# Kernel tuning notes

Measured on AMD Instinct MI355X. Metric: run time of the kernel, lower is better.

## Reference

```python
import jax, jax.numpy as jnp
import numpy as np

N = 100000
MAX_HOPS = 3
EPS = 1e-16


def _gat_conv(x, src, dst, W, a_src, a_dst, bias, heads, out_c, concat):
    """PyG-style GATConv (eval mode, self-loops, negative_slope=0.2)."""
    n = x.shape[0]
    loop = jnp.arange(n, dtype=src.dtype)
    s = jnp.concatenate([src, loop])
    d = jnp.concatenate([dst, loop])
    h = (x @ W).reshape(n, heads, out_c)                      # [N,H,C]
    al_s = (h * a_src).sum(-1)                                # [N,H]
    al_d = (h * a_dst).sum(-1)                                # [N,H]
    e = jax.nn.leaky_relu(al_s[s] + al_d[d], 0.2)             # [E,H]
    e_max = jax.ops.segment_max(e, d, num_segments=n)
    e = jnp.exp(e - e_max[d])
    denom = jax.ops.segment_sum(e, d, num_segments=n)
    alpha = e / (denom[d] + EPS)                              # edge softmax per dst
    out = jax.ops.segment_sum(h[s] * alpha[:, :, None], d, num_segments=n)  # [N,H,C]
    out = out.reshape(n, heads * out_c) if concat else out.mean(axis=1)
    return out + bias


def _hierarchy(src, dst, seed, n, max_hops):
    """BFS hop distance from seeds; one-hot rows, all-zero if unreached."""
    reached = seed
    dist = jnp.where(seed, 0, max_hops + 1)
    for h in range(1, max_hops + 1):
        msg = jax.ops.segment_max(reached[src].astype(jnp.int32), dst, num_segments=n)
        nbr = msg > 0
        dist = jnp.where(nbr & (~reached), h, dist)
        reached = reached | nbr
    mask = (dist[:, None] == jnp.arange(max_hops + 1)[None, :]).astype(jnp.float32)
    hop_counts = jnp.argmax(mask, axis=1).astype(jnp.float32)  # all-zero row -> 0, like torch
    return mask, hop_counts


def setup_inputs() -> dict:
    key = jax.random.key(0)
    ks = jax.random.split(key, 20)
    in_aug = 128 + MAX_HOPS + 1  # 132
    out_channels = 40
    g = lambda k, shp: (jax.random.normal(k, shp, dtype=jnp.float32) * 0.1)
    return {
        "x": jax.random.normal(ks[0], (N, 128), dtype=jnp.float32),
        "edge_index": jax.random.randint(ks[1], (2, 1600000), 0, N, dtype=jnp.int64),
        "seed_mask": jax.random.randint(ks[2], (N,), 0, 100, dtype=jnp.int32),
        "W1": g(ks[3], (in_aug, 8 * 8)), "a1s": g(ks[4], (8, 8)), "a1d": g(ks[5], (8, 8)), "b1": jnp.zeros((64,), jnp.float32),
        "W2": g(ks[6], (64, 8 * 16)), "a2s": g(ks[7], (8, 16)), "a2d": g(ks[8], (8, 16)), "b2": jnp.zeros((128,), jnp.float32),
        "W3": g(ks[9], (128, out_channels)), "a3s": g(ks[10], (1, out_channels)), "a3d": g(ks[11], (1, out_channels)), "b3": jnp.zeros((out_channels,), jnp.float32),
        "Wg": g(ks[12], (129, 1)), "bg": jnp.zeros((1,), jnp.float32),
    }


def reference(x, edge_index, seed_mask, W1, a1s, a1d, b1, W2, a2s, a2d, b2,
              W3, a3s, a3d, b3, Wg, bg):
    src, dst = edge_index[0], edge_index[1]
    seed = seed_mask == 0
    hmask, hop_counts = _hierarchy(src, dst, seed, N, MAX_HOPS)
    aug = jnp.concatenate([x, hmask], axis=1)
    h1 = jax.nn.elu(_gat_conv(aug, src, dst, W1, a1s, a1d, b1, 8, 8, True))
    h2 = _gat_conv(h1, src, dst, W2, a2s, a2d, b2, 8, 16, True)
    gate_in = jnp.concatenate([h2, hop_counts[:, None]], axis=1)
    gate = jax.nn.sigmoid(gate_in @ Wg + bg)
    h2 = h2 * gate
    h3 = _gat_conv(h2, src, dst, W3, a3s, a3d, b3, 1, 40, False)
    return jax.nn.log_softmax(h3, axis=1)
```

## Files before the change

### kernel.cpp

```cpp
#include <hip/hip_runtime.h>
#include <hip/hip_bf16.h>
#include <hip/hip_fp16.h>
#include <math.h>

#define MAXH 3
#define NSB 8
#define NS (1 << NSB)
#define SRCBITS 17
#define SRCMASK ((1 << SRCBITS) - 1)
#define LOG2E 1.4426950408889634f
typedef unsigned int u32;
typedef unsigned long long u64;
typedef unsigned char u8;
typedef unsigned short u16;

using bf16x8 = __attribute__((ext_vector_type(8))) short;
using f32x4  = __attribute__((ext_vector_type(4))) float;

__device__ __forceinline__ float fexp2(float x) {
#if __has_builtin(__builtin_amdgcn_exp2f)
    return __builtin_amdgcn_exp2f(x);
#else
    return exp2f(x);
#endif
}
__device__ __forceinline__ u16 f2bf(float f) {
    u32 u = __float_as_uint(f);
    u32 r = ((u >> 16) & 1u) + 0x7fffu;
    return (u16)((u + r) >> 16);
}

__global__ void k_init(const int* __restrict__ seed_mask, int* dist, u64* rb64,
                       int* bincnt, int n) {
    int i = blockIdx.x * 256 + threadIdx.x;
    int lane = threadIdx.x & 63;
    bool seed = (i < n) && (seed_mask[i] == 0);
    if (i < n) dist[i] = seed ? 0 : (MAXH + 1);
    u64 b = __ballot(seed);
    if (lane == 0 && (i & ~63) < n) rb64[i >> 6] = b;
    if (blockIdx.x == 0) {
        bincnt[threadIdx.x] = 0;
        bincnt[threadIdx.x + 256] = 0;
    }
}

__global__ void k_bfs_step(const int* __restrict__ rowptr, const int* __restrict__ csr_src,
                           const u32* __restrict__ rbOld, u64* rbNew, int* dist,
                           int h, int n) {
    int i = blockIdx.x * 256 + threadIdx.x;
    int lane = threadIdx.x & 63;
    bool reached = false;
    if (i < n) {
        reached = (rbOld[i >> 5] >> (i & 31)) & 1u;
        if (!reached) {
            int beg = rowptr[i], end = rowptr[i + 1];
            for (int k = beg; k < end; k++) {
                int s = csr_src[k];
                if ((rbOld[s >> 5] >> (s & 31)) & 1u) { reached = true; dist[i] = h; break; }
            }
        }
    }
    u64 b = __ballot(reached);
    if (lane == 0 && (i & ~63) < n) rbNew[i >> 6] = b;
}

__global__ void k_bincount(const int4* __restrict__ dst4, int* bincnt, int E4) {
    __shared__ int cnt[512];
    int t = threadIdx.x;
    cnt[t] = 0; cnt[t + 256] = 0;
    __syncthreads();
    int i = blockIdx.x * 256 + t;
    if (i < E4) {
        int4 d = dst4[i];
        atomicAdd(&cnt[d.x >> NSB], 1);
        atomicAdd(&cnt[d.y >> NSB], 1);
        atomicAdd(&cnt[d.z >> NSB], 1);
        atomicAdd(&cnt[d.w >> NSB], 1);
    }
    __syncthreads();
    if (cnt[t] > 0) atomicAdd(&bincnt[t], cnt[t]);
    if (cnt[t + 256] > 0) atomicAdd(&bincnt[t + 256], cnt[t + 256]);
}

__global__ void k_binscan(const int* __restrict__ bincnt, int* binbase, int* bincur,
                          int* rowptr, int BINS, int E, int n) {
    __shared__ int sd[512];
    int t = threadIdx.x;
    int v = (t < BINS) ? bincnt[t] : 0;
    sd[t] = v;
    __syncthreads();
    for (int off = 1; off < 512; off <<= 1) {
        int add = (t >= off) ? sd[t - off] : 0;
        __syncthreads();
        sd[t] += add;
        __syncthreads();
    }
    int excl = sd[t] - v;
    if (t < BINS) { binbase[t] = excl; bincur[t] = excl; }
    if (t == 0) { binbase[BINS] = E; rowptr[n] = E; }
}

__global__ void k_binscatter(const int4* __restrict__ src4, const int4* __restrict__ dst4,
                             int* bincur, int* __restrict__ pairs, int E4, int BINS) {
    __shared__ int cnt[512], base[512];
    int t = threadIdx.x;
    cnt[t] = 0; cnt[t + 256] = 0;
    __syncthreads();
    int i = blockIdx.x * 256 + t;
    int bin[4], rank[4], pack[4];
    bool valid = i < E4;
    if (valid) {
        int4 s = src4[i], d = dst4[i];
        bin[0] = d.x >> NSB; pack[0] = ((d.x & (NS - 1)) << SRCBITS) | s.x;
        bin[1] = d.y >> NSB; pack[1] = ((d.y & (NS - 1)) << SRCBITS) | s.y;
        bin[2] = d.z >> NSB; pack[2] = ((d.z & (NS - 1)) << SRCBITS) | s.z;
        bin[3] = d.w >> NSB; pack[3] = ((d.w & (NS - 1)) << SRCBITS) | s.w;
        rank[0] = atomicAdd(&cnt[bin[0]], 1);
        rank[1] = atomicAdd(&cnt[bin[1]], 1);
        rank[2] = atomicAdd(&cnt[bin[2]], 1);
        rank[3] = atomicAdd(&cnt[bin[3]], 1);
    }
    __syncthreads();
    if (cnt[t] > 0) base[t] = atomicAdd(&bincur[t], cnt[t]);
    if (cnt[t + 256] > 0) base[t + 256] = atomicAdd(&bincur[t + 256], cnt[t + 256]);
    __syncthreads();
    if (valid) {
        pairs[base[bin[0]] + rank[0]] = pack[0];
        pairs[base[bin[1]] + rank[1]] = pack[1];
        pairs[base[bin[2]] + rank[2]] = pack[2];
        pairs[base[bin[3]] + rank[3]] = pack[3];
    }
}

__global__ void k_binsort(const int* __restrict__ pairs, const int* __restrict__ binbase,
                          int* __restrict__ rowptr, int* __restrict__ csr_src, int n) {
    __shared__ int hist[NS];
    const int b = blockIdx.x, t = threadIdx.x;
    const int nbeg = b << NSB;
    const int ebeg = binbase[b];
    const int ecnt = binbase[b + 1] - ebeg;
    hist[t] = 0;
    __syncthreads();
    for (int i = t; i < ecnt; i += 256)
        atomicAdd(&hist[(u32)pairs[ebeg + i] >> SRCBITS], 1);
    for (int d = 1; d < NS; d <<= 1) {
        __syncthreads();
        int idx = (t + 1) * (d << 1) - 1;
        if (idx < NS) hist[idx] += hist[idx - d];
    }
    __syncthreads();
    if (t == 0) hist[NS - 1] = 0;
    for (int d = NS / 2; d >= 1; d >>= 1) {
        __syncthreads();
        int idx = (t + 1) * (d << 1) - 1;
        if (idx < NS) { int tmp = hist[idx - d]; hist[idx - d] = hist[idx]; hist[idx] += tmp; }
    }
    __syncthreads();
    int g0 = nbeg + t;
    if (g0 < n) rowptr[g0] = ebeg + hist[t];
    __syncthreads();
    for (int i = t; i < ecnt; i += 256) {
        int p = pairs[ebeg + i];
        int pos = atomicAdd(&hist[(u32)p >> SRCBITS], 1);
        csr_src[ebeg + pos] = p & SRCMASK;
    }
}

template <int SK, int MBW>
__launch_bounds__(256)
__global__ void k_gemm_mfma1(const float* __restrict__ A, const float* __restrict__ W,
                             const float* __restrict__ a_s, const float* __restrict__ a_d,
                             const int* __restrict__ dist, __half* __restrict__ out,
                             float* __restrict__ als, float* __restrict__ ald, int n) {
    constexpr int K = 128, NREAL = 64, NTT = 5, AH = 8, C = 8;
    constexpr int KT = K / 32;
    constexpr int NTCOL = (NTT - 1) * 16;
    __shared__ u16 WT[NTT * 16 * SK];
    __shared__ u16 sAW[4][16 * SK];
    __shared__ float sAug[4][64];
    __shared__ float sAugA[4][16];

    for (int idx = threadIdx.x; idx < NTT * 16 * K; idx += 256) {
        int c = idx / K, k = idx % K;
        float v;
        if (c < NREAL) {
            v = W[k * NREAL + c];
        } else {
            int j = (c - NTCOL) & 7;
            const float* aw = (c < NTCOL + AH) ? a_s : a_d;
            float accv = 0.0f;
            for (int cc = 0; cc < C; cc++) accv += W[k * NREAL + j * C + cc] * aw[j * C + cc];
            v = accv * LOG2E;
        }
        WT[c * SK + k] = f2bf(v);
    }
    {
        int t = threadIdx.x;
        int d = t >> 6, c = t & 63;
        sAug[d][c] = W[(K + d) * NREAL + c];
        if (t < 64) {
            int dd = t >> 4, j = t & 15;
            int hh = j & 7;
            const float* aw = (j < 8) ? a_s : a_d;
            float accv = 0.0f;
            for (int cc = 0; cc < C; cc++)
                accv += W[(K + dd) * NREAL + hh * C + cc] * aw[hh * C + cc];
            sAugA[dd][j] = accv * LOG2E;
        }
    }
    __syncthreads();

    const int lane = threadIdx.x & 63;
    const int l15 = lane & 15;
    const int kg = lane >> 4;
    const int w = threadIdx.x >> 6;
    const int wid = blockIdx.x * 4 + w;

    bf16x8 bfr[NTT][KT];
#pragma unroll
    for (int nt = 0; nt < NTT; nt++)
#pragma unroll
        for (int kt = 0; kt < KT; kt++)
            bfr[nt][kt] = *(const bf16x8*)&WT[(nt * 16 + l15) * SK + kt * 32 + kg * 8];

    for (int mb = 0; mb < MBW; mb++) {
        const int rowbase = (wid * MBW + mb) * 16;
        if (rowbase >= n) break;
        {
            int r = lane >> 2, c4b = lane & 3;
            const float* xr = A + (size_t)(rowbase + r) * K;
#pragma unroll
            for (int j = 0; j < 8; j++) {
                int c4 = c4b + j * 4;
                float4 v = *(const float4*)&xr[c4 * 4];
                ushort4 o;
                o.x = f2bf(v.x); o.y = f2bf(v.y); o.z = f2bf(v.z); o.w = f2bf(v.w);
                *(ushort4*)&sAW[w][r * SK + c4 * 4] = o;
            }
        }
        bf16x8 af[KT];
#pragma unroll
        for (int kt = 0; kt < KT; kt++)
            af[kt] = *(const bf16x8*)&sAW[w][l15 * SK + kt * 32 + kg * 8];
        f32x4 acc[NTT];
#pragma unroll
        for (int nt = 0; nt < NTT; nt++) acc[nt] = f32x4{0.f, 0.f, 0.f, 0.f};
#pragma unroll
        for (int kt = 0; kt < KT; kt++)
#pragma unroll
            for (int nt = 0; nt < NTT; nt++)
                acc[nt] = __builtin_amdgcn_mfma_f32_16x16x32_bf16(af[kt], bfr[nt][kt],
                                                                  acc[nt], 0, 0, 0);
        int rows[4], dd[4];
#pragma unroll
        for (int r = 0; r < 4; r++) {
            rows[r] = rowbase + kg * 4 + r;
            dd[r] = dist[rows[r]];
        }
#pragma unroll
        for (int nt = 0; nt < NTT - 1; nt++) {
            int c = nt * 16 + l15;
#pragma unroll
            for (int r = 0; r < 4; r++) {
                float v = acc[nt][r];
                if (dd[r] <= MAXH) v += sAug[dd[r]][c];
                out[(size_t)rows[r] * NREAL + c] = __float2half(v);
            }
        }
#pragma unroll
        for (int r = 0; r < 4; r++) {
            float v = acc[NTT - 1][r];
            if (dd[r] <= MAXH) v += sAugA[dd[r]][l15];
            if (l15 < AH) als[(size_t)rows[r] * AH + l15] = v;
            else ald[(size_t)rows[r] * AH + (l15 - AH)] = v;
        }
    }
}

template <int K, int NREAL, int NTT, int AH, int C, int SK, int MBW>
__launch_bounds__(256)
__global__ void k_gemm_mfma(const u16* __restrict__ A, const float* __restrict__ W,
                            const float* __restrict__ a_s, const float* __restrict__ a_d,
                            __half* __restrict__ out, float* __restrict__ als,
                            float* __restrict__ ald, int n) {
    constexpr int KT = K / 32;
    constexpr int NTCOL = (NTT - 1) * 16;
    __shared__ u16 WT[NTT * 16 * SK];
    for (int idx = threadIdx.x; idx < NTT * 16 * K; idx += 256) {
        int c = idx / K, k = idx % K;
        float v = 0.0f;
        if (c < NREAL) {
            v = W[k * NREAL + c];
        } else if (c >= NTCOL && c < NTCOL + 2 * AH) {
            int j = (c - NTCOL) % AH;
            const float* aw = (c < NTCOL + AH) ? a_s : a_d;
            float accv = 0.0f;
            for (int cc = 0; cc < C; cc++) accv += W[k * NREAL + j * C + cc] * aw[j * C + cc];
            v = accv * LOG2E;
        }
        WT[c * SK + k] = f2bf(v);
    }
    __syncthreads();

    const int lane = threadIdx.x & 63;
    const int l15 = lane & 15;
    const int kg = lane >> 4;
    const int wid = blockIdx.x * 4 + (threadIdx.x >> 6);

    bf16x8 bfr[NTT][KT];
#pragma unroll
    for (int nt = 0; nt < NTT; nt++)
#pragma unroll
        for (int kt = 0; kt < KT; kt++)
            bfr[nt][kt] = *(const bf16x8*)&WT[(nt * 16 + l15) * SK + kt * 32 + kg * 8];

    for (int mb = 0; mb < MBW; mb++) {
        const int rowbase = (wid * MBW + mb) * 16;
        if (rowbase >= n) break;
        bf16x8 af[KT];
#pragma unroll
        for (int kt = 0; kt < KT; kt++)
            af[kt] = *(const bf16x8*)&A[(size_t)(rowbase + l15) * K + kt * 32 + kg * 8];
        f32x4 acc[NTT];
#pragma unroll
        for (int nt = 0; nt < NTT; nt++) acc[nt] = f32x4{0.f, 0.f, 0.f, 0.f};
#pragma unroll
        for (int kt = 0; kt < KT; kt++)
#pragma unroll
            for (int nt = 0; nt < NTT; nt++)
                acc[nt] = __builtin_amdgcn_mfma_f32_16x16x32_bf16(af[kt], bfr[nt][kt],
                                                                  acc[nt], 0, 0, 0);
#pragma unroll
        for (int nt = 0; nt < NTT - 1; nt++) {
            int c = nt * 16 + l15;
            if (c < NREAL) {
#pragma unroll
                for (int r = 0; r < 4; r++) {
                    int row = rowbase + kg * 4 + r;
                    out[(size_t)row * NREAL + c] = __float2half(acc[nt][r]);
                }
            }
        }
#pragma unroll
        for (int r = 0; r < 4; r++) {
            int row = rowbase + kg * 4 + r;
            float v = acc[NTT - 1][r];
            if (l15 < AH) als[(size_t)row * AH + l15] = v;
            else if (l15 < 2 * AH) ald[(size_t)row * AH + (l15 - AH)] = v;
        }
    }
}

template <int H, int C, int CH, int MODE, typename OT>
__launch_bounds__(1024)
__global__ void k_gat(const int* __restrict__ rowptr, const int* __restrict__ csr_src,
                      const __half* __restrict__ h, const float* __restrict__ als,
                      const float* __restrict__ ald, const float* __restrict__ bias,
                      const int* __restrict__ dist, const float* __restrict__ Wg,
                      const float* __restrict__ bg, OT* __restrict__ out, int n) {
    constexpr int TOT = H * C;
    constexpr int NL = TOT / CH;
    const int lane = threadIdx.x & 63;
    const int node = blockIdx.x * 16 + (threadIdx.x >> 6);
    if (node >= n) return;
    const int beg = rowptr[node];
    const int deg = rowptr[node + 1] - beg;

    const int cl = (lane < NL) ? lane : 0;
    const int hd = (cl * CH) / C;
    const float ald_hd = ald[(size_t)node * H + hd];
    const float t0 = als[(size_t)node * H + hd] + ald_hd;
    const float m0 = fmaxf(t0, 0.2f * t0);
    const float c0 = ald_hd - m0;
    const float c1 = 0.2f * ald_hd - m0;

    float s = 1.0f;
    float ax = 0.0f, ay = 0.0f;
    __half2 acc2;
    if (MODE == 2) {
        acc2 = *(const __half2*)(h + (size_t)node * TOT + cl * 2);
    } else {
        ax = __half2float(h[(size_t)node * TOT + cl]);
    }

    auto body = [&](int sN) {
        float a = als[(size_t)sN * H + hd];
        float v = fmaxf(a + c0, fmaf(a, 0.2f, c1));
        float p = fexp2(v);
        s += p;
        if (MODE == 2) {
            __half2 ph = __float2half2_rn(p);
            acc2 = __hfma2(ph, *(const __half2*)(h + (size_t)sN * TOT + cl * 2), acc2);
        } else {
            ax += p * __half2float(h[(size_t)sN * TOT + cl]);
        }
    };

    for (int base = 0; base < deg; base += 64) {
        const int myE = base + lane;
        int sReg = (myE < deg) ? csr_src[beg + myE] : 0;
        const int cnt = min(64, deg - base);
        int e = 0;
        for (; e + 4 <= cnt; e += 4) {
            body(__builtin_amdgcn_readlane(sReg, e));
            body(__builtin_amdgcn_readlane(sReg, e + 1));
            body(__builtin_amdgcn_readlane(sReg, e + 2));
            body(__builtin_amdgcn_readlane(sReg, e + 3));
        }
        for (; e < cnt; e++) body(__builtin_amdgcn_readlane(sReg, e));
    }

    const float inv = 1.0f / (s + 1e-16f);
    if (MODE == 2) {
        float2 av = __half22float2(acc2);
        ax = av.x; ay = av.y;
    }
    float vx = ax * inv + bias[cl * CH];
    float vy = (CH == 2) ? (ay * inv + bias[cl * CH + 1]) : 0.0f;

    if (MODE == 1) {
        vx = vx > 0.0f ? vx : expm1f(vx);
        ((u16*)out)[(size_t)node * TOT + cl] = f2bf(vx);
    } else if (MODE == 2) {
        float2 wg = *(const float2*)&Wg[cl * 2];
        float part = vx * wg.x + vy * wg.y;
#pragma unroll
        for (int off = 32; off > 0; off >>= 1) part += __shfl_xor(part, off);
        int d = dist[node];
        float hop = (d <= MAXH) ? (float)d : 0.0f;
        float g = 1.0f / (1.0f + __expf(-(part + hop * Wg[128] + bg[0])));
        ushort2 wv;
        wv.x = f2bf(vx * g);
        wv.y = f2bf(vy * g);
        *(ushort2*)&((u16*)out)[(size_t)node * TOT + cl * 2] = wv;
    } else if (MODE == 3) {
        float v = (lane < NL) ? vx : -INFINITY;
        float mm = v;
#pragma unroll
        for (int off = 32; off > 0; off >>= 1) mm = fmaxf(mm, __shfl_xor(mm, off));
        float ex = (lane < NL) ? __expf(v - mm) : 0.0f;
        float ss = ex;
#pragma unroll
        for (int off = 32; off > 0; off >>= 1) ss += __shfl_xor(ss, off);
        float ls = logf(ss);
        if (lane < NL) ((float*)out)[(size_t)node * TOT + cl] = v - mm - ls;
    }
}

static inline int nblk(long long t, int b) { return (int)((t + b - 1) / b); }

extern "C" void kernel_launch(void* const* d_in, const int* in_sizes, int n_in,
                              void* d_out, int out_size, void* d_ws, size_t ws_size,
                              hipStream_t stream) {
    const float* x = (const float*)d_in[0];
    const int* eidx = (const int*)d_in[1];
    const int* seed_mask = (const int*)d_in[2];
    const float* W1 = (const float*)d_in[3];
    const float* a1s = (const float*)d_in[4];
    const float* a1d = (const float*)d_in[5];
    const float* b1 = (const float*)d_in[6];
    const float* W2 = (const float*)d_in[7];
    const float* a2s = (const float*)d_in[8];
    const float* a2d = (const float*)d_in[9];
    const float* b2 = (const float*)d_in[10];
    const float* W3 = (const float*)d_in[11];
    const float* a3s = (const float*)d_in[12];
    const float* a3d = (const float*)d_in[13];
    const float* b3 = (const float*)d_in[14];
    const float* Wg = (const float*)d_in[15];
    const float* bg = (const float*)d_in[16];

    const int n = in_sizes[0] / 128;
    const long long E = in_sizes[1] / 2;
    const int E4 = (int)(E / 4);
    const int4* src4 = (const int4*)eidx;
    const int4* dst4 = (const int4*)(eidx + E);
    const int BINS = (n + NS - 1) >> NSB;
    const int NW64 = (n + 63) / 64;

    char* ws = (char*)d_ws;
    size_t off = 0;
    auto alloc = [&](size_t bytes) -> void* {
        void* p = ws + off;
        off = (off + bytes + 255) & ~(size_t)255;
        return p;
    };
    int* dist    = (int*)alloc((size_t)n * 4);
    u64* rbA     = (u64*)alloc((size_t)NW64 * 8);
    u64* rbB     = (u64*)alloc((size_t)NW64 * 8);
    int* rowptr  = (int*)alloc((size_t)(n + 1) * 4);
    int* bincnt  = (int*)alloc(512 * 4);
    int* binbase = (int*)alloc(513 * 4);
    int* bincur  = (int*)alloc(512 * 4);
    int* csr_src = (int*)alloc((size_t)E * 4);
    float* als   = (float*)alloc((size_t)n * 8 * 4);
    float* ald   = (float*)alloc((size_t)n * 8 * 4);
    __half* hbuf = (__half*)alloc((size_t)n * 128 * 2);
    u16* abuf    = (u16*)alloc((size_t)n * 128 * 2);
    int* pairs   = (int*)abuf;
    float* out = (float*)d_out;

    const int BS = 256;

    k_init<<<nblk(n, BS), BS, 0, stream>>>(seed_mask, dist, rbA, bincnt, n);

    k_bincount<<<nblk(E4, BS), BS, 0, stream>>>(dst4, bincnt, E4);
    k_binscan<<<1, 512, 0, stream>>>(bincnt, binbase, bincur, rowptr, BINS, (int)E, n);
    k_binscatter<<<nblk(E4, BS), BS, 0, stream>>>(src4, dst4, bincur, pairs, E4, BINS);
    k_binsort<<<BINS, 256, 0, stream>>>(pairs, binbase, rowptr, csr_src, n);

    k_bfs_step<<<nblk(n, BS), BS, 0, stream>>>(rowptr, csr_src, (const u32*)rbA, rbB,
                                               dist, 1, n);
    k_bfs_step<<<nblk(n, BS), BS, 0, stream>>>(rowptr, csr_src, (const u32*)rbB, rbA,
                                               dist, 2, n);
    k_bfs_step<<<nblk(n, BS), BS, 0, stream>>>(rowptr, csr_src, (const u32*)rbA, rbB,
                                               dist, 3, n);

    const int mblocks = (n + 15) / 16;
    const int gmf = (mblocks + 15) / 16;

    k_gemm_mfma1<136, 4>
        <<<gmf, 256, 0, stream>>>(x, W1, a1s, a1d, dist, hbuf, als, ald, n);
    k_gat<8, 8, 1, 1, u16><<<nblk(n, 16), 1024, 0, stream>>>(
        rowptr, csr_src, hbuf, als, ald, b1, nullptr, nullptr, nullptr, abuf, n);

    k_gemm_mfma<64, 128, 9, 8, 16, 72, 4>
        <<<gmf, 256, 0, stream>>>(abuf, W2, a2s, a2d, hbuf, als, ald, n);
    k_gat<8, 16, 2, 2, u16><<<nblk(n, 16), 1024, 0, stream>>>(
        rowptr, csr_src, hbuf, als, ald, b2, dist, Wg, bg, abuf, n);

    k_gemm_mfma<128, 40, 4, 1, 40, 136, 4>
        <<<gmf, 256, 0, stream>>>(abuf, W3, a3s, a3d, hbuf, als, ald, n);
    k_gat<1, 40, 1, 3, float><<<nblk(n, 16), 1024, 0, stream>>>(
        rowptr, csr_src, hbuf, als, ald, b3, nullptr, nullptr, nullptr, out, n);
}
```

Measured before the change: 441.5 us.

## Process multiple edges per wavefront in GAT aggregation with wider per-lane channels

The GAT aggregation kernel now splits each 64-lane wavefront into edge groups (2 or 3) so that idle lanes process different neighbor edges concurrently. Each lane also handles 2 or 4 channels with vector loads, and partial sums are combined across groups with shuffles before the epilogue. Block size drops from 1024 to 256 threads with launch bounds set for higher occupancy. The binscatter kernel moves to 1024-thread blocks to reduce global atomics on the bin cursors. Extra shuffle reductions and predicated invalid edges add some overhead.

```diff
diff --git a/kernel.cpp b/kernel.cpp
--- a/kernel.cpp
+++ b/kernel.cpp
@@ -100,13 +100,14 @@
     if (t == 0) { binbase[BINS] = E; rowptr[n] = E; }
 }
 
+__launch_bounds__(1024)
 __global__ void k_binscatter(const int4* __restrict__ src4, const int4* __restrict__ dst4,
                              int* bincur, int* __restrict__ pairs, int E4, int BINS) {
     __shared__ int cnt[512], base[512];
     int t = threadIdx.x;
-    cnt[t] = 0; cnt[t + 256] = 0;
-    __syncthreads();
-    int i = blockIdx.x * 256 + t;
+    if (t < 512) cnt[t] = 0;
+    __syncthreads();
+    int i = blockIdx.x * 1024 + t;
     int bin[4], rank[4], pack[4];
     bool valid = i < E4;
     if (valid) {
@@ -121,8 +122,7 @@
         rank[3] = atomicAdd(&cnt[bin[3]], 1);
     }
     __syncthreads();
-    if (cnt[t] > 0) base[t] = atomicAdd(&bincur[t], cnt[t]);
-    if (cnt[t + 256] > 0) base[t + 256] = atomicAdd(&bincur[t + 256], cnt[t + 256]);
+    if (t < 512 && cnt[t] > 0) base[t] = atomicAdd(&bincur[t], cnt[t]);
     __syncthreads();
     if (valid) {
         pairs[base[bin[0]] + rank[0]] = pack[0];
@@ -351,8 +351,8 @@
     }
 }
 
-template <int H, int C, int CH, int MODE, typename OT>
-__launch_bounds__(1024)
+template <int H, int C, int CH, int EPP, int MODE, typename OT>
+__launch_bounds__(256, 8)
 __global__ void k_gat(const int* __restrict__ rowptr, const int* __restrict__ csr_src,
                       const __half* __restrict__ h, const float* __restrict__ als,
                       const float* __restrict__ ald, const float* __restrict__ bias,
@@ -361,12 +361,13 @@
     constexpr int TOT = H * C;
     constexpr int NL = TOT / CH;
     const int lane = threadIdx.x & 63;
-    const int node = blockIdx.x * 16 + (threadIdx.x >> 6);
+    const int node = blockIdx.x * 4 + (threadIdx.x >> 6);
     if (node >= n) return;
     const int beg = rowptr[node];
     const int deg = rowptr[node + 1] - beg;
 
-    const int cl = (lane < NL) ? lane : 0;
+    const int eg = lane / NL;
+    const int cl = lane % NL;
     const int hd = (cl * CH) / C;
     const float ald_hd = ald[(size_t)node * H + hd];
     const float t0 = als[(size_t)node * H + hd] + ald_hd;
@@ -374,76 +375,129 @@
     const float c0 = ald_hd - m0;
     const float c1 = 0.2f * ald_hd - m0;
 
-    float s = 1.0f;
+    float s = (eg == 0) ? 1.0f : 0.0f;
     float ax = 0.0f, ay = 0.0f;
-    __half2 acc2;
-    if (MODE == 2) {
-        acc2 = *(const __half2*)(h + (size_t)node * TOT + cl * 2);
-    } else {
-        ax = __half2float(h[(size_t)node * TOT + cl]);
-    }
-
-    auto body = [&](int sN) {
+    __half2 accLo = __floats2half2_rn(0.f, 0.f), accHi = accLo;
+    if (eg == 0) {
+        if (MODE == 2) {
+            uint2 hv = *(const uint2*)(h + (size_t)node * TOT + cl * CH);
+            accLo = *(const __half2*)&hv.x;
+            accHi = *(const __half2*)&hv.y;
+        } else {
+            float2 hf = __half22float2(*(const __half2*)(h + (size_t)node * TOT + cl * CH));
+            ax = hf.x; ay = hf.y;
+        }
+    }
+
+    auto body = [&](int sN, bool valid) {
         float a = als[(size_t)sN * H + hd];
         float v = fmaxf(a + c0, fmaf(a, 0.2f, c1));
-        float p = fexp2(v);
+        float p = valid ? fexp2(v) : 0.0f;
         s += p;
         if (MODE == 2) {
             __half2 ph = __float2half2_rn(p);
-            acc2 = __hfma2(ph, *(const __half2*)(h + (size_t)sN * TOT + cl * 2), acc2);
+            uint2 hv = *(const uint2*)(h + (size_t)sN * TOT + cl * CH);
+            accLo = __hfma2(ph, *(const __half2*)&hv.x, accLo);
+            accHi = __hfma2(ph, *(const __half2*)&hv.y, accHi);
         } else {
-            ax += p * __half2float(h[(size_t)sN * TOT + cl]);
-        }
+            float2 hf = __half22float2(*(const __half2*)(h + (size_t)sN * TOT + cl * CH));
+            ax += p * hf.x;
+            ay += p * hf.y;
+        }
+    };
+
+    auto group = [&](int sReg, int e0, int cnt) {
+        int sN;
+        if (EPP == 2) {
+            int s0 = __builtin_amdgcn_readlane(sReg, e0);
+            int s1 = __builtin_amdgcn_readlane(sReg, e0 + 1);
+            sN = eg ? s1 : s0;
+        } else {
+            int s0 = __builtin_amdgcn_readlane(sReg, e0);
+            int s1 = __builtin_amdgcn_readlane(sReg, min(e0 + 1, 63));
+            int s2 = __builtin_amdgcn_readlane(sReg, min(e0 + 2, 63));
+            sN = (eg == 0) ? s0 : ((eg == 1) ? s1 : s2);
+        }
+        bool valid = (eg < EPP) && (e0 + eg < cnt);
+        body(sN, valid);
     };
 
     for (int base = 0; base < deg; base += 64) {
         const int myE = base + lane;
         int sReg = (myE < deg) ? csr_src[beg + myE] : 0;
         const int cnt = min(64, deg - base);
-        int e = 0;
-        for (; e + 4 <= cnt; e += 4) {
-            body(__builtin_amdgcn_readlane(sReg, e));
-            body(__builtin_amdgcn_readlane(sReg, e + 1));
-            body(__builtin_amdgcn_readlane(sReg, e + 2));
-            body(__builtin_amdgcn_readlane(sReg, e + 3));
-        }
-        for (; e < cnt; e++) body(__builtin_amdgcn_readlane(sReg, e));
-    }
-
+        const int ng = (cnt + EPP - 1) / EPP;
+        int it = 0;
+        for (; it + 2 <= ng; it += 2) {
+            group(sReg, it * EPP, cnt);
+            group(sReg, (it + 1) * EPP, cnt);
+        }
+        for (; it < ng; it++) group(sReg, it * EPP, cnt);
+    }
+
+    if (EPP == 2) {
+        s += __shfl_xor(s, 32);
+        if (MODE == 2) {
+            int lo = __shfl_xor(*(int*)&accLo, 32);
+            int hi = __shfl_xor(*(int*)&accHi, 32);
+            accLo = __hadd2(accLo, *(const __half2*)&lo);
+            accHi = __hadd2(accHi, *(const __half2*)&hi);
+        } else {
+            ax += __shfl_xor(ax, 32);
+            ay += __shfl_xor(ay, 32);
+        }
+    } else {
+        float sa = __shfl(s, lane + 20), sb = __shfl(s, lane + 40);
+        float xa = __shfl(ax, lane + 20), xb = __shfl(ax, lane + 40);
+        float ya = __shfl(ay, lane + 20), yb = __shfl(ay, lane + 40);
+        s += sa + sb; ax += xa + xb; ay += ya + yb;
+    }
+
+    const bool wlane = (lane < NL);
     const float inv = 1.0f / (s + 1e-16f);
-    if (MODE == 2) {
-        float2 av = __half22float2(acc2);
-        ax = av.x; ay = av.y;
-    }
-    float vx = ax * inv + bias[cl * CH];
-    float vy = (CH == 2) ? (ay * inv + bias[cl * CH + 1]) : 0.0f;
 
     if (MODE == 1) {
-        vx = vx > 0.0f ? vx : expm1f(vx);
-        ((u16*)out)[(size_t)node * TOT + cl] = f2bf(vx);
+        if (wlane) {
+            float vx = ax * inv + bias[cl * 2];
+            float vy = ay * inv + bias[cl * 2 + 1];
+            vx = vx > 0.0f ? vx : expm1f(vx);
+            vy = vy > 0.0f ? vy : expm1f(vy);
+            ushort2 wv; wv.x = f2bf(vx); wv.y = f2bf(vy);
+            *(ushort2*)&((u16*)out)[(size_t)node * TOT + cl * 2] = wv;
+        }
     } else if (MODE == 2) {
-        float2 wg = *(const float2*)&Wg[cl * 2];
-        float part = vx * wg.x + vy * wg.y;
-#pragma unroll
-        for (int off = 32; off > 0; off >>= 1) part += __shfl_xor(part, off);
+        float2 lo = __half22float2(accLo), hi = __half22float2(accHi);
+        float v0 = lo.x * inv + bias[cl * 4];
+        float v1 = lo.y * inv + bias[cl * 4 + 1];
+        float v2 = hi.x * inv + bias[cl * 4 + 2];
+        float v3 = hi.y * inv + bias[cl * 4 + 3];
+        float4 wg = *(const float4*)&Wg[cl * 4];
+        float part = v0 * wg.x + v1 * wg.y + v2 * wg.z + v3 * wg.w;
+#pragma unroll
+        for (int off = 16; off > 0; off >>= 1) part += __shfl_xor(part, off);
         int d = dist[node];
         float hop = (d <= MAXH) ? (float)d : 0.0f;
         float g = 1.0f / (1.0f + __expf(-(part + hop * Wg[128] + bg[0])));
-        ushort2 wv;
-        wv.x = f2bf(vx * g);
-        wv.y = f2bf(vy * g);
-        *(ushort2*)&((u16*)out)[(size_t)node * TOT + cl * 2] = wv;
-    } else if (MODE == 3) {
-        float v = (lane < NL) ? vx : -INFINITY;
-        float mm = v;
-#pragma unroll
-        for (int off = 32; off > 0; off >>= 1) mm = fmaxf(mm, __shfl_xor(mm, off));
-        float ex = (lane < NL) ? __expf(v - mm) : 0.0f;
-        float ss = ex;
-#pragma unroll
-        for (int off = 32; off > 0; off >>= 1) ss += __shfl_xor(ss, off);
-        float ls = logf(ss);
-        if (lane < NL) ((float*)out)[(size_t)node * TOT + cl] = v - mm - ls;
+        if (wlane) {
+            ushort4 wv;
+            wv.x = f2bf(v0 * g); wv.y = f2bf(v1 * g);
+            wv.z = f2bf(v2 * g); wv.w = f2bf(v3 * g);
+            *(ushort4*)&((u16*)out)[(size_t)node * TOT + cl * 4] = wv;
+        }
+    } else {
+        float vx = ax * inv + bias[cl * 2];
+        float vy = ay * inv + bias[cl * 2 + 1];
+        float mval = wlane ? fmaxf(vx, vy) : -INFINITY;
+#pragma unroll
+        for (int off = 16; off > 0; off >>= 1) mval = fmaxf(mval, __shfl_xor(mval, off));
+        float ex = wlane ? __expf(vx - mval) + __expf(vy - mval) : 0.0f;
+#pragma unroll
+        for (int off = 16; off > 0; off >>= 1) ex += __shfl_xor(ex, off);
+        float ls = logf(ex);
+        if (wlane) {
+            *(float2*)&((float*)out)[(size_t)node * TOT + cl * 2] =
+                float2{vx - mval - ls, vy - mval - ls};
+        }
     }
 }
 
@@ -506,7 +560,7 @@
 
     k_bincount<<<nblk(E4, BS), BS, 0, stream>>>(dst4, bincnt, E4);
     k_binscan<<<1, 512, 0, stream>>>(bincnt, binbase, bincur, rowptr, BINS, (int)E, n);
-    k_binscatter<<<nblk(E4, BS), BS, 0, stream>>>(src4, dst4, bincur, pairs, E4, BINS);
+    k_binscatter<<<nblk(E4, 1024), 1024, 0, stream>>>(src4, dst4, bincur, pairs, E4, BINS);
     k_binsort<<<BINS, 256, 0, stream>>>(pairs, binbase, rowptr, csr_src, n);
 
     k_bfs_step<<<nblk(n, BS), BS, 0, stream>>>(rowptr, csr_src, (const u32*)rbA, rbB,
@@ -521,16 +575,16 @@
 
     k_gemm_mfma1<136, 4>
         <<<gmf, 256, 0, stream>>>(x, W1, a1s, a1d, dist, hbuf, als, ald, n);
-    k_gat<8, 8, 1, 1, u16><<<nblk(n, 16), 1024, 0, stream>>>(
+    k_gat<8, 8, 2, 2, 1, u16><<<nblk(n, 4), 256, 0, stream>>>(
         rowptr, csr_src, hbuf, als, ald, b1, nullptr, nullptr, nullptr, abuf, n);
 
     k_gemm_mfma<64, 128, 9, 8, 16, 72, 4>
         <<<gmf, 256, 0, stream>>>(abuf, W2, a2s, a2d, hbuf, als, ald, n);
-    k_gat<8, 16, 2, 2, u16><<<nblk(n, 16), 1024, 0, stream>>>(
+    k_gat<8, 16, 4, 2, 2, u16><<<nblk(n, 4), 256, 0, stream>>>(
         rowptr, csr_src, hbuf, als, ald, b2, dist, Wg, bg, abuf, n);
 
     k_gemm_mfma<128, 40, 4, 1, 40, 136, 4>
         <<<gmf, 256, 0, stream>>>(abuf, W3, a3s, a3d, hbuf, als, ald, n);
-    k_gat<1, 40, 1, 3, float><<<nblk(n, 16), 1024, 0, stream>>>(
+    k_gat<1, 40, 2, 3, 3, float><<<nblk(n, 4), 256, 0, stream>>>(
         rowptr, csr_src, hbuf, als, ald, b3, nullptr, nullptr, nullptr, out, n);
 }
```

Measured after the change: 361.5 us. 18.1% less time.
